# Kernel tuning notes

Hardware: AMD Instinct MI355X
Metric: run time of the kernel (lower is better)

## Reference

```python
import jax, jax.numpy as jnp
import numpy as np

WBITS = 4
GROUP_SIZE = 64
QMAX = 2 ** WBITS - 1  # 15
EPS = 1e-5


def setup_inputs() -> dict:
    key = jax.random.key(0)
    k1, k2, k3 = jax.random.split(key, 3)
    x = jax.random.normal(k1, (1, 512, 11008), dtype=jnp.float32)
    weight = jax.random.normal(k2, (4096, 11008), dtype=jnp.float32) * 0.02
    bias = jax.random.normal(k3, (4096,), dtype=jnp.float32) * 0.02
    return {"x": x, "weight": weight, "bias": bias}


def fake_quant_groupwise(w: jnp.ndarray) -> jnp.ndarray:
    """Uniform affine (asymmetric) group-wise fake quantization of the weight.

    Groups of GROUP_SIZE contiguous elements along the flattened weight share
    one (scale, zero_point) pair, computed dynamically from min/max per group,
    as in UniformAffineQuantizer(wbits, group_size, weight).
    """
    orig_shape = w.shape
    wg = w.reshape(-1, GROUP_SIZE)                     # [n_groups, G]
    xmin = jnp.min(wg, axis=1, keepdims=True)          # [n_groups, 1]
    xmax = jnp.max(wg, axis=1, keepdims=True)
    scale = jnp.maximum(xmax - xmin, EPS) / QMAX       # [n_groups, 1]
    zero_point = jnp.round(-xmin / scale)              # [n_groups, 1]
    w_int = jnp.clip(jnp.round(wg / scale) + zero_point, 0, QMAX)
    w_dq = (w_int - zero_point) * scale
    return w_dq.reshape(orig_shape)


def reference(x, weight, bias):
    w_q = fake_quant_groupwise(weight)                 # [out, in]
    # F.linear: x @ w_q.T + bias
    out = jnp.einsum('bsi,oi->bso', x, w_q) + bias
    return out
```

## Files before the change

kernel.cpp:

```cpp
#include <hip/hip_runtime.h>
#include <hip/hip_bf16.h>
#include <stdint.h>

typedef __attribute__((ext_vector_type(8))) short bf16x8;
typedef __attribute__((ext_vector_type(8))) short short8;
typedef __attribute__((ext_vector_type(4))) float f32x4;

#define M_DIM 512
#define N_DIM 4096
#define K_DIM 11008
#define KSTEPS 172

#define GLOBAL_AS(p) ((const __attribute__((address_space(1))) void*)(p))
#define LDS_AS(p)    ((__attribute__((address_space(3))) void*)(p))

__device__ __forceinline__ short f2bf(float f) {
    unsigned u = __float_as_uint(f);
    unsigned r = u + 0x7fff + ((u >> 16) & 1);
    return (short)(r >> 16);
}

__device__ __forceinline__ unsigned cvt_pk_bf16(float lo, float hi) {
    unsigned r;
    asm("v_cvt_pk_bf16_f32 %0, %1, %2" : "=v"(r) : "v"(lo), "v"(hi));
    return r;
}

__device__ __forceinline__ void fence_bar() {
    asm volatile("" ::: "memory");
    __builtin_amdgcn_s_barrier();
    asm volatile("" ::: "memory");
}
#define LGKM0() asm volatile("s_waitcnt lgkmcnt(0)" ::: "memory")
#define VMCNT(n) asm volatile("s_waitcnt vmcnt(" #n ")" ::: "memory")

__global__ __launch_bounds__(256) void conv_x(const float* __restrict__ x, short* __restrict__ xb) {
    const long long total = (long long)M_DIM * K_DIM;
    for (long long e0 = ((long long)blockIdx.x * 256 + threadIdx.x) * 8;
         e0 < total;
         e0 += (long long)gridDim.x * 256 * 8) {
        const float4* p = (const float4*)(x + e0);
        float4 v0 = p[0];
        float4 v1 = p[1];
        short8 s;
        s[0] = f2bf(v0.x); s[1] = f2bf(v0.y); s[2] = f2bf(v0.z); s[3] = f2bf(v0.w);
        s[4] = f2bf(v1.x); s[5] = f2bf(v1.y); s[6] = f2bf(v1.z); s[7] = f2bf(v1.w);
        *(short8*)(xb + e0) = s;
    }
}


template<int QD>
__device__ __forceinline__ void phase_reads(const short* __restrict__ Asd,
                                            const short* __restrict__ Bsd,
                                            int arow, int brow, int qb,
                                            bf16x8 (&af)[2][2], bf16x8 (&bfr)[2][4]) {
    if (QD == 0) {
        #pragma unroll
        for (int ks = 0; ks < 2; ++ks)
            #pragma unroll
            for (int fn = 0; fn < 4; ++fn) {
                const int r = brow + fn * 16;
                bfr[ks][fn] = *(const bf16x8*)&Bsd[r * 64 + (((ks * 4 + qb) ^ (r & 7)) * 8)];
            }
    }
    #pragma unroll
    for (int ks = 0; ks < 2; ++ks)
        #pragma unroll
        for (int j = 0; j < 2; ++j) {
            const int r = arow + (QD * 2 + j) * 16;
            af[ks][j] = *(const bf16x8*)&Asd[r * 64 + (((ks * 4 + qb) ^ (r & 7)) * 8)];
        }
}

template<int QD>
__device__ __forceinline__ void phase_mfma(const bf16x8 (&af)[2][2], const bf16x8 (&bfr)[2][4],
                                           f32x4 (&acc)[8][4]) {
    __builtin_amdgcn_s_setprio(1);
    #pragma unroll
    for (int ks = 0; ks < 2; ++ks)
        #pragma unroll
        for (int j = 0; j < 2; ++j)
            #pragma unroll
            for (int fn = 0; fn < 4; ++fn)
                acc[QD * 2 + j][fn] = __builtin_amdgcn_mfma_f32_16x16x32_bf16(
                    af[ks][j], bfr[ks][fn], acc[QD * 2 + j][fn], 0, 0, 0);
    __builtin_amdgcn_s_setprio(0);
}

__global__ __launch_bounds__(512, 2) void gemm_fq(const short* __restrict__ A,
                                                  const float* __restrict__ W,
                                                  unsigned short* __restrict__ P,
                                                  int spb) {
    __shared__ short As[2][256 * 64];
    __shared__ short Bs[2][256 * 64];
    const int tid  = threadIdx.x;
    const int lane = tid & 63;
    const int w    = tid >> 6;
    const int wr   = w >> 2;
    const int wc   = w & 3;
    const int m0   = blockIdx.y * 256;
    const int n0   = blockIdx.x * 256;
    const int kt0  = blockIdx.z * spb;
    const int kt1  = min(kt0 + spb, KSTEPS);

    const int srow = tid >> 3;
    const int sswz = (tid & 7) ^ (srow & 7);
    const int rQ   = tid >> 3;
    const int sQ   = tid & 7;
    const int arow = wr * 128 + (lane & 15);
    const int brow = wc * 64 + (lane & 15);
    const int qb   = lane >> 4;

    f32x4  acc[8][4] = {};
    bf16x8 bfr[2][4];
    bf16x8 af[2][2];
    float4 c0[2], c1[2], c2[2], c3[2];

    auto stageA = [&](int d, int h, int kt) {
        #pragma unroll
        for (int l = 0; l < 2; ++l) {
            __builtin_amdgcn_global_load_lds(
                GLOBAL_AS(A + (size_t)(m0 + h * 128 + l * 64 + srow) * K_DIM + kt * 64 + sswz * 8),
                LDS_AS(&As[d][(h * 128 + l * 64 + w * 8) * 64]), 16, 0, 0);
        }
    };
    auto loadBq = [&](float4 (&dst)[2], int c, int kt) {
        const float* src = W + (size_t)(n0 + c * 64 + rQ) * K_DIM + kt * 64 + sQ * 8;
        dst[0] = *(const float4*)(src);
        dst[1] = *(const float4*)(src + 4);
    };
    auto quantC = [&](const float4 (&v)[2], int c, short* BsF) {
        float mn = fminf(fminf(fminf(v[0].x, v[0].y), fminf(v[0].z, v[0].w)),
                         fminf(fminf(v[1].x, v[1].y), fminf(v[1].z, v[1].w)));
        float mx = fmaxf(fmaxf(fmaxf(v[0].x, v[0].y), fmaxf(v[0].z, v[0].w)),
                         fmaxf(fmaxf(v[1].x, v[1].y), fmaxf(v[1].z, v[1].w)));
        mn = fminf(mn, __int_as_float(__builtin_amdgcn_mov_dpp(__float_as_int(mn), 0xB1, 0xf, 0xf, true)));
        mx = fmaxf(mx, __int_as_float(__builtin_amdgcn_mov_dpp(__float_as_int(mx), 0xB1, 0xf, 0xf, true)));
        mn = fminf(mn, __int_as_float(__builtin_amdgcn_mov_dpp(__float_as_int(mn), 0x4E, 0xf, 0xf, true)));
        mx = fmaxf(mx, __int_as_float(__builtin_amdgcn_mov_dpp(__float_as_int(mx), 0x4E, 0xf, 0xf, true)));
        mn = fminf(mn, __int_as_float(__builtin_amdgcn_ds_swizzle(__float_as_int(mn), 0x101F)));
        mx = fmaxf(mx, __int_as_float(__builtin_amdgcn_ds_swizzle(__float_as_int(mx), 0x101F)));
        float range = fmaxf(mx - mn, 1e-5f);
        float scale = range * (1.0f / 15.0f);
        float rs    = 15.0f / range;
        float zp    = rintf(-mn * rs);
        const float lo = -zp, hi = 15.0f - zp;
        const float* pv = (const float*)&v[0];
        float q[8];
        #pragma unroll
        for (int j = 0; j < 8; ++j)
            q[j] = fminf(fmaxf(rintf(pv[j] * rs), lo), hi) * scale;
        union { unsigned u[4]; short8 s; } pk;
        #pragma unroll
        for (int j = 0; j < 4; ++j)
            pk.u[j] = cvt_pk_bf16(q[2 * j], q[2 * j + 1]);
        const int r = c * 64 + rQ;
        *(short8*)&BsF[r * 64 + ((sQ ^ (r & 7)) * 8)] = pk.s;
    };

    loadBq(c0, 0, kt0); loadBq(c1, 1, kt0); loadBq(c2, 2, kt0); loadBq(c3, 3, kt0);
    stageA(0, 0, kt0); stageA(0, 1, kt0);
    VMCNT(10); quantC(c0, 0, Bs[0]);
    VMCNT(8);  quantC(c1, 1, Bs[0]);
    VMCNT(6);  quantC(c2, 2, Bs[0]);
    VMCNT(4);  quantC(c3, 3, Bs[0]);
    {
        const int t1 = kt0 + 1;
        loadBq(c0, 0, t1); loadBq(c1, 1, t1); loadBq(c2, 2, t1); loadBq(c3, 3, t1);
    }
    VMCNT(8);
    VMCNT(6);
    LGKM0();
    fence_bar();

    int par = 0;
    for (int t = kt0; t < kt1; ++t) {
        const int tn  = (t + 1 < kt1) ? t + 1 : t;
        const int tn2 = (t + 2 < kt1) ? t + 2 : kt1 - 1;
        const short* Asc = As[par];
        const short* Bsc = Bs[par];
        short* Bsn = Bs[par ^ 1];
        phase_reads<0>(Asc, Bsc, arow, brow, qb, af, bfr);
        quantC(c0, 0, Bsn);
        stageA(par ^ 1, 0, tn);
        loadBq(c0, 0, tn2);
        fence_bar(); LGKM0();
        phase_mfma<0>(af, bfr, acc);
        fence_bar();
        phase_reads<1>(Asc, Bsc, arow, brow, qb, af, bfr);
        VMCNT(8);
        quantC(c1, 1, Bsn);
        stageA(par ^ 1, 1, tn);
        loadBq(c1, 1, tn2);
        fence_bar(); LGKM0();
        phase_mfma<1>(af, bfr, acc);
        fence_bar();
        phase_reads<2>(Asc, Bsc, arow, brow, qb, af, bfr);
        VMCNT(10);
        quantC(c2, 2, Bsn);
        loadBq(c2, 2, tn2);
        fence_bar(); LGKM0();
        phase_mfma<2>(af, bfr, acc);
        fence_bar();
        phase_reads<3>(Asc, Bsc, arow, brow, qb, af, bfr);
        VMCNT(10);
        quantC(c3, 3, Bsn);
        loadBq(c3, 3, tn2);
        fence_bar(); LGKM0();
        phase_mfma<3>(af, bfr, acc);
        VMCNT(6);
        fence_bar();
        par ^= 1;
    }

    VMCNT(0);

    unsigned short* out = P + (size_t)blockIdx.z * M_DIM * N_DIM;
    #pragma unroll
    for (int fm = 0; fm < 8; ++fm) {
        #pragma unroll
        for (int fn = 0; fn < 4; ++fn) {
            const int col  = n0 + wc * 64 + fn * 16 + (lane & 15);
            const int rowb = m0 + wr * 128 + fm * 16 + (lane >> 4) * 4;
            #pragma unroll
            for (int r = 0; r < 4; ++r) {
                out[(size_t)(rowb + r) * N_DIM + col] = (unsigned short)f2bf(acc[fm][fn][r]);
            }
        }
    }
}

__global__ __launch_bounds__(256) void reduce_out(const unsigned short* __restrict__ P,
                                                  const float* __restrict__ bias,
                                                  float* __restrict__ out,
                                                  int splitk) {
    const size_t total = (size_t)M_DIM * N_DIM;
    for (size_t idx8 = ((size_t)blockIdx.x * 256 + threadIdx.x) * 8;
         idx8 < total;
         idx8 += (size_t)gridDim.x * 256 * 8) {
        const int col = (int)(idx8 % N_DIM);
        float s[8];
        {
            float4 b0 = *(const float4*)(bias + col);
            float4 b1 = *(const float4*)(bias + col + 4);
            s[0] = b0.x; s[1] = b0.y; s[2] = b0.z; s[3] = b0.w;
            s[4] = b1.x; s[5] = b1.y; s[6] = b1.z; s[7] = b1.w;
        }
        for (int sp = 0; sp < splitk; ++sp) {
            short8 p = *(const short8*)(P + (size_t)sp * total + idx8);
            #pragma unroll
            for (int j = 0; j < 8; ++j)
                s[j] += __uint_as_float(((unsigned)(unsigned short)p[j]) << 16);
        }
        float4 o0 = {s[0], s[1], s[2], s[3]};
        float4 o1 = {s[4], s[5], s[6], s[7]};
        *(float4*)(out + idx8) = o0;
        *(float4*)(out + idx8 + 4) = o1;
    }
}

extern "C" void kernel_launch(void* const* d_in, const int* in_sizes, int n_in,
                              void* d_out, int out_size, void* d_ws, size_t ws_size,
                              hipStream_t stream) {
    const float* x    = (const float*)d_in[0];
    const float* wgt  = (const float*)d_in[1];
    const float* bias = (const float*)d_in[2];
    float* out = (float*)d_out;

    char* ws = (char*)d_ws;
    const size_t xb_bytes = (size_t)M_DIM * K_DIM * 2;
    short* xb = (short*)ws;
    unsigned short* part = (unsigned short*)(ws + xb_bytes);

    const size_t per_split = (size_t)M_DIM * N_DIM * 2;
    size_t avail = (ws_size > xb_bytes) ? (ws_size - xb_bytes) : 0;
    int splitk = 1, spb = KSTEPS;
    for (int sk = 8; sk >= 1; --sk) {
        if ((size_t)sk * per_split > avail) continue;
        int s = (KSTEPS + sk - 1) / sk;
        if (s & 1) s++;
        int last = KSTEPS - (sk - 1) * s;
        if (last < 2) continue;
        splitk = sk; spb = s;
        break;
    }

    hipLaunchKernelGGL(conv_x, dim3(2048), dim3(256), 0, stream, x, xb);
    hipLaunchKernelGGL(gemm_fq, dim3(N_DIM / 256, M_DIM / 256, splitk), dim3(512), 0, stream,
                       xb, wgt, part, spb);
    hipLaunchKernelGGL(reduce_out, dim3(1024), dim3(256), 0, stream, part, bias, out, splitk);
}
```

Before: 90.02 us.

## Remap weight quantization to two threads per row with register-level min/max

Each thread now loads 32 contiguous weight floats (half a 64-element group) instead of 8 floats across four chunks, so the group min/max reduction happens mostly in registers and needs a single DPP exchange instead of DPP plus ds_swizzle. The main loop is unrolled by two with fixed LDS buffer indices, and weight loads, reductions and quantization are spread over phases differently. This cuts cross-lane reduction work and gives wider contiguous loads. In exchange, register pressure rises (16 float4 buffers), and the wait-count and odd-step handling in the 2x unrolled loop are more fragile.

```diff
diff --git a/kernel.cpp b/kernel.cpp
--- a/kernel.cpp
+++ b/kernel.cpp
@@ -24,6 +24,15 @@
     unsigned r;
     asm("v_cvt_pk_bf16_f32 %0, %1, %2" : "=v"(r) : "v"(lo), "v"(hi));
     return r;
+}
+
+__device__ __forceinline__ float dpp_xor1_min(float v) {
+    int r = __builtin_amdgcn_mov_dpp(__float_as_int(v), 0xB1, 0xf, 0xf, true);
+    return fminf(v, __int_as_float(r));
+}
+__device__ __forceinline__ float dpp_xor1_max(float v) {
+    int r = __builtin_amdgcn_mov_dpp(__float_as_int(v), 0xB1, 0xf, 0xf, true);
+    return fmaxf(v, __int_as_float(r));
 }
 
 __device__ __forceinline__ void fence_bar() {
@@ -106,8 +115,8 @@
 
     const int srow = tid >> 3;
     const int sswz = (tid & 7) ^ (srow & 7);
-    const int rQ   = tid >> 3;
-    const int sQ   = tid & 7;
+    const int rQ   = tid >> 1;
+    const int hQ   = tid & 1;
     const int arow = wr * 128 + (lane & 15);
     const int brow = wc * 64 + (lane & 15);
     const int qb   = lane >> 4;
@@ -115,7 +124,8 @@
     f32x4  acc[8][4] = {};
     bf16x8 bfr[2][4];
     bf16x8 af[2][2];
-    float4 c0[2], c1[2], c2[2], c3[2];
+    float4 R0[8], R1[8];
+    float scale, rs, zp, qlo, qhi;
 
     auto stageA = [&](int d, int h, int kt) {
         #pragma unroll
@@ -125,93 +135,125 @@
                 LDS_AS(&As[d][(h * 128 + l * 64 + w * 8) * 64]), 16, 0, 0);
         }
     };
-    auto loadBq = [&](float4 (&dst)[2], int c, int kt) {
-        const float* src = W + (size_t)(n0 + c * 64 + rQ) * K_DIM + kt * 64 + sQ * 8;
-        dst[0] = *(const float4*)(src);
-        dst[1] = *(const float4*)(src + 4);
+    auto loadR = [&](float4 (&dst)[8], int half, int kt) {
+        const float4* src = (const float4*)(W + (size_t)(n0 + rQ) * K_DIM + kt * 64 + hQ * 32 + half * 16);
+        #pragma unroll
+        for (int j = 0; j < 4; ++j) dst[half * 4 + j] = src[j];
     };
-    auto quantC = [&](const float4 (&v)[2], int c, short* BsF) {
-        float mn = fminf(fminf(fminf(v[0].x, v[0].y), fminf(v[0].z, v[0].w)),
-                         fminf(fminf(v[1].x, v[1].y), fminf(v[1].z, v[1].w)));
-        float mx = fmaxf(fmaxf(fmaxf(v[0].x, v[0].y), fmaxf(v[0].z, v[0].w)),
-                         fmaxf(fmaxf(v[1].x, v[1].y), fmaxf(v[1].z, v[1].w)));
-        mn = fminf(mn, __int_as_float(__builtin_amdgcn_mov_dpp(__float_as_int(mn), 0xB1, 0xf, 0xf, true)));
-        mx = fmaxf(mx, __int_as_float(__builtin_amdgcn_mov_dpp(__float_as_int(mx), 0xB1, 0xf, 0xf, true)));
-        mn = fminf(mn, __int_as_float(__builtin_amdgcn_mov_dpp(__float_as_int(mn), 0x4E, 0xf, 0xf, true)));
-        mx = fmaxf(mx, __int_as_float(__builtin_amdgcn_mov_dpp(__float_as_int(mx), 0x4E, 0xf, 0xf, true)));
-        mn = fminf(mn, __int_as_float(__builtin_amdgcn_ds_swizzle(__float_as_int(mn), 0x101F)));
-        mx = fmaxf(mx, __int_as_float(__builtin_amdgcn_ds_swizzle(__float_as_int(mx), 0x101F)));
+    auto reduceR = [&](const float4 (&R)[8]) {
+        float mns[8], mxs[8];
+        #pragma unroll
+        for (int i = 0; i < 8; ++i) {
+            mns[i] = fminf(fminf(R[i].x, R[i].y), fminf(R[i].z, R[i].w));
+            mxs[i] = fmaxf(fmaxf(R[i].x, R[i].y), fmaxf(R[i].z, R[i].w));
+        }
+        #pragma unroll
+        for (int st = 4; st >= 1; st >>= 1)
+            #pragma unroll
+            for (int i = 0; i < st; ++i) {
+                mns[i] = fminf(mns[i], mns[i + st]);
+                mxs[i] = fmaxf(mxs[i], mxs[i + st]);
+            }
+        float mn = dpp_xor1_min(mns[0]);
+        float mx = dpp_xor1_max(mxs[0]);
         float range = fmaxf(mx - mn, 1e-5f);
-        float scale = range * (1.0f / 15.0f);
-        float rs    = 15.0f / range;
-        float zp    = rintf(-mn * rs);
-        const float lo = -zp, hi = 15.0f - zp;
-        const float* pv = (const float*)&v[0];
-        float q[8];
-        #pragma unroll
-        for (int j = 0; j < 8; ++j)
-            q[j] = fminf(fmaxf(rintf(pv[j] * rs), lo), hi) * scale;
-        union { unsigned u[4]; short8 s; } pk;
-        #pragma unroll
-        for (int j = 0; j < 4; ++j)
-            pk.u[j] = cvt_pk_bf16(q[2 * j], q[2 * j + 1]);
-        const int r = c * 64 + rQ;
-        *(short8*)&BsF[r * 64 + ((sQ ^ (r & 7)) * 8)] = pk.s;
+        scale = range * (1.0f / 15.0f);
+        rs    = 1.0f / scale;
+        zp    = rintf(-mn * rs);
+        qlo   = -zp;
+        qhi   = 15.0f - zp;
     };
-
-    loadBq(c0, 0, kt0); loadBq(c1, 1, kt0); loadBq(c2, 2, kt0); loadBq(c3, 3, kt0);
+    auto quantHalf = [&](const float4 (&R)[8], int half16, short* BsF) {
+        #pragma unroll
+        for (int pairq = 0; pairq < 2; ++pairq) {
+            const float4 va = R[half16 * 4 + pairq * 2 + 0];
+            const float4 vb = R[half16 * 4 + pairq * 2 + 1];
+            float q[8];
+            const float* pv = (const float*)&va;
+            #pragma unroll
+            for (int j = 0; j < 4; ++j)
+                q[j] = fminf(fmaxf(rintf(pv[j] * rs), qlo), qhi) * scale;
+            pv = (const float*)&vb;
+            #pragma unroll
+            for (int j = 0; j < 4; ++j)
+                q[4 + j] = fminf(fmaxf(rintf(pv[j] * rs), qlo), qhi) * scale;
+            union { unsigned u[4]; short8 s; } pk;
+            #pragma unroll
+            for (int j = 0; j < 4; ++j)
+                pk.u[j] = cvt_pk_bf16(q[2 * j], q[2 * j + 1]);
+            const int s = hQ * 4 + half16 * 2 + pairq;
+            *(short8*)&BsF[rQ * 64 + ((s ^ (rQ & 7)) * 8)] = pk.s;
+        }
+    };
+
+    loadR(R0, 0, kt0); loadR(R0, 1, kt0);
     stageA(0, 0, kt0); stageA(0, 1, kt0);
-    VMCNT(10); quantC(c0, 0, Bs[0]);
-    VMCNT(8);  quantC(c1, 1, Bs[0]);
-    VMCNT(6);  quantC(c2, 2, Bs[0]);
-    VMCNT(4);  quantC(c3, 3, Bs[0]);
-    {
-        const int t1 = kt0 + 1;
-        loadBq(c0, 0, t1); loadBq(c1, 1, t1); loadBq(c2, 2, t1); loadBq(c3, 3, t1);
-    }
+    VMCNT(4);
+    reduceR(R0);
+    quantHalf(R0, 0, Bs[0]);
+    quantHalf(R0, 1, Bs[0]);
+    loadR(R1, 0, kt0 + 1); loadR(R1, 1, kt0 + 1);
     VMCNT(8);
-    VMCNT(6);
     LGKM0();
     fence_bar();
 
-    int par = 0;
-    for (int t = kt0; t < kt1; ++t) {
-        const int tn  = (t + 1 < kt1) ? t + 1 : t;
-        const int tn2 = (t + 2 < kt1) ? t + 2 : kt1 - 1;
-        const short* Asc = As[par];
-        const short* Bsc = Bs[par];
-        short* Bsn = Bs[par ^ 1];
-        phase_reads<0>(Asc, Bsc, arow, brow, qb, af, bfr);
-        quantC(c0, 0, Bsn);
-        stageA(par ^ 1, 0, tn);
-        loadBq(c0, 0, tn2);
+    for (int t = kt0; t < kt1; t += 2) {
+        const int tb  = t + 1;
+        const int ta2 = (t + 2 < kt1) ? t + 2 : kt1 - 1;
+        const int tb2 = (t + 3 < kt1) ? t + 3 : kt1 - 1;
+        const int tAn = (t + 2 < kt1) ? t + 2 : tb;
+
+        phase_reads<0>(As[0], Bs[0], arow, brow, qb, af, bfr);
+        VMCNT(0);
+        reduceR(R1);
+        stageA(1, 0, tb);
+        loadR(R0, 0, ta2);
         fence_bar(); LGKM0();
         phase_mfma<0>(af, bfr, acc);
         fence_bar();
-        phase_reads<1>(Asc, Bsc, arow, brow, qb, af, bfr);
-        VMCNT(8);
-        quantC(c1, 1, Bsn);
-        stageA(par ^ 1, 1, tn);
-        loadBq(c1, 1, tn2);
+        phase_reads<1>(As[0], Bs[0], arow, brow, qb, af, bfr);
+        quantHalf(R1, 0, Bs[1]);
+        stageA(1, 1, tb);
+        loadR(R0, 1, ta2);
         fence_bar(); LGKM0();
         phase_mfma<1>(af, bfr, acc);
         fence_bar();
-        phase_reads<2>(Asc, Bsc, arow, brow, qb, af, bfr);
-        VMCNT(10);
-        quantC(c2, 2, Bsn);
-        loadBq(c2, 2, tn2);
+        phase_reads<2>(As[0], Bs[0], arow, brow, qb, af, bfr);
+        quantHalf(R1, 1, Bs[1]);
         fence_bar(); LGKM0();
         phase_mfma<2>(af, bfr, acc);
         fence_bar();
-        phase_reads<3>(Asc, Bsc, arow, brow, qb, af, bfr);
-        VMCNT(10);
-        quantC(c3, 3, Bsn);
-        loadBq(c3, 3, tn2);
+        phase_reads<3>(As[0], Bs[0], arow, brow, qb, af, bfr);
         fence_bar(); LGKM0();
         phase_mfma<3>(af, bfr, acc);
-        VMCNT(6);
-        fence_bar();
-        par ^= 1;
+        VMCNT(4);
+        fence_bar();
+
+        phase_reads<0>(As[1], Bs[1], arow, brow, qb, af, bfr);
+        VMCNT(0);
+        reduceR(R0);
+        stageA(0, 0, tAn);
+        loadR(R1, 0, tb2);
+        fence_bar(); LGKM0();
+        phase_mfma<0>(af, bfr, acc);
+        fence_bar();
+        phase_reads<1>(As[1], Bs[1], arow, brow, qb, af, bfr);
+        quantHalf(R0, 0, Bs[0]);
+        stageA(0, 1, tAn);
+        loadR(R1, 1, tb2);
+        fence_bar(); LGKM0();
+        phase_mfma<1>(af, bfr, acc);
+        fence_bar();
+        phase_reads<2>(As[1], Bs[1], arow, brow, qb, af, bfr);
+        quantHalf(R0, 1, Bs[0]);
+        fence_bar(); LGKM0();
+        phase_mfma<2>(af, bfr, acc);
+        fence_bar();
+        phase_reads<3>(As[1], Bs[1], arow, brow, qb, af, bfr);
+        fence_bar(); LGKM0();
+        phase_mfma<3>(af, bfr, acc);
+        VMCNT(4);
+        fence_bar();
     }
 
     VMCNT(0);
```

Result: slower. 171.4 us (+90.4%).

## Shrink GEMM tile to 128x128 with single-stage B quantization per k-step

Applied to the files above, without the earlier changes.

Rewrites the fused fake-quant GEMM to use 128x128 tiles with 256 threads. Each thread now loads 32 weights, and a pair of lanes reduces the group min/max. The four-phase interleaved pipeline becomes a simpler per-k-step loop with one B buffer. Split-K changes from up to 8 to 4. Doubling the number of M tiles means the fp32 weight is re-read and re-quantized twice as often, and the shallower pipeline hides less latency.

```diff
diff --git a/kernel.cpp b/kernel.cpp
--- a/kernel.cpp
+++ b/kernel.cpp
@@ -24,6 +24,10 @@
     unsigned r;
     asm("v_cvt_pk_bf16_f32 %0, %1, %2" : "=v"(r) : "v"(lo), "v"(hi));
     return r;
+}
+
+__device__ __forceinline__ float dpp_xor1(float v) {
+    return __int_as_float(__builtin_amdgcn_mov_dpp(__float_as_int(v), 0xB1, 0xf, 0xf, true));
 }
 
 __device__ __forceinline__ void fence_bar() {
@@ -49,167 +53,121 @@
     }
 }
 
-
-template<int QD>
-__device__ __forceinline__ void phase_reads(const short* __restrict__ Asd,
-                                            const short* __restrict__ Bsd,
-                                            int arow, int brow, int qb,
-                                            bf16x8 (&af)[2][2], bf16x8 (&bfr)[2][4]) {
-    if (QD == 0) {
-        #pragma unroll
-        for (int ks = 0; ks < 2; ++ks)
-            #pragma unroll
-            for (int fn = 0; fn < 4; ++fn) {
-                const int r = brow + fn * 16;
-                bfr[ks][fn] = *(const bf16x8*)&Bsd[r * 64 + (((ks * 4 + qb) ^ (r & 7)) * 8)];
-            }
-    }
-    #pragma unroll
-    for (int ks = 0; ks < 2; ++ks)
-        #pragma unroll
-        for (int j = 0; j < 2; ++j) {
-            const int r = arow + (QD * 2 + j) * 16;
-            af[ks][j] = *(const bf16x8*)&Asd[r * 64 + (((ks * 4 + qb) ^ (r & 7)) * 8)];
-        }
-}
-
-template<int QD>
-__device__ __forceinline__ void phase_mfma(const bf16x8 (&af)[2][2], const bf16x8 (&bfr)[2][4],
-                                           f32x4 (&acc)[8][4]) {
-    __builtin_amdgcn_s_setprio(1);
-    #pragma unroll
-    for (int ks = 0; ks < 2; ++ks)
-        #pragma unroll
-        for (int j = 0; j < 2; ++j)
-            #pragma unroll
-            for (int fn = 0; fn < 4; ++fn)
-                acc[QD * 2 + j][fn] = __builtin_amdgcn_mfma_f32_16x16x32_bf16(
-                    af[ks][j], bfr[ks][fn], acc[QD * 2 + j][fn], 0, 0, 0);
-    __builtin_amdgcn_s_setprio(0);
-}
-
-__global__ __launch_bounds__(512, 2) void gemm_fq(const short* __restrict__ A,
+__global__ __launch_bounds__(256, 2) void gemm_fq(const short* __restrict__ A,
                                                   const float* __restrict__ W,
                                                   unsigned short* __restrict__ P,
                                                   int spb) {
-    __shared__ short As[2][256 * 64];
-    __shared__ short Bs[2][256 * 64];
+    __shared__ short As[2][128 * 64];
+    __shared__ short Bs[128 * 64];
     const int tid  = threadIdx.x;
     const int lane = tid & 63;
     const int w    = tid >> 6;
-    const int wr   = w >> 2;
-    const int wc   = w & 3;
-    const int m0   = blockIdx.y * 256;
-    const int n0   = blockIdx.x * 256;
+    const int wr   = w >> 1;
+    const int wc   = w & 1;
+    const int m0   = blockIdx.y * 128;
+    const int n0   = blockIdx.x * 128;
     const int kt0  = blockIdx.z * spb;
     const int kt1  = min(kt0 + spb, KSTEPS);
 
-    const int srow = tid >> 3;
-    const int sswz = (tid & 7) ^ (srow & 7);
-    const int rQ   = tid >> 3;
-    const int sQ   = tid & 7;
-    const int arow = wr * 128 + (lane & 15);
-    const int brow = wc * 64 + (lane & 15);
+    const int srow = lane >> 3;
+    const int slot = lane & 7;
+    const int rQ   = tid >> 1;
+    const int hQ   = tid & 1;
+    const int frA  = wr * 64 + (lane & 15);
+    const int frB  = wc * 64 + (lane & 15);
     const int qb   = lane >> 4;
 
-    f32x4  acc[8][4] = {};
-    bf16x8 bfr[2][4];
-    bf16x8 af[2][2];
-    float4 c0[2], c1[2], c2[2], c3[2];
-
-    auto stageA = [&](int d, int h, int kt) {
-        #pragma unroll
-        for (int l = 0; l < 2; ++l) {
+    f32x4  acc[4][4] = {};
+    float4 R[8];
+
+    auto stageA = [&](int d, int kt) {
+        #pragma unroll
+        for (int i = 0; i < 4; ++i) {
+            const int rb  = (w * 4 + i) * 8;
+            const int row = rb + srow;
+            const int gcol = ((slot ^ (row & 7)) * 8);
             __builtin_amdgcn_global_load_lds(
-                GLOBAL_AS(A + (size_t)(m0 + h * 128 + l * 64 + srow) * K_DIM + kt * 64 + sswz * 8),
-                LDS_AS(&As[d][(h * 128 + l * 64 + w * 8) * 64]), 16, 0, 0);
+                GLOBAL_AS(A + (size_t)(m0 + row) * K_DIM + kt * 64 + gcol),
+                LDS_AS(&As[d][rb * 64]), 16, 0, 0);
         }
     };
-    auto loadBq = [&](float4 (&dst)[2], int c, int kt) {
-        const float* src = W + (size_t)(n0 + c * 64 + rQ) * K_DIM + kt * 64 + sQ * 8;
-        dst[0] = *(const float4*)(src);
-        dst[1] = *(const float4*)(src + 4);
+    auto loadR = [&](int kt) {
+        const float4* src = (const float4*)(W + (size_t)(n0 + rQ) * K_DIM + (size_t)kt * 64 + hQ * 32);
+        #pragma unroll
+        for (int j = 0; j < 8; ++j) R[j] = src[j];
     };
-    auto quantC = [&](const float4 (&v)[2], int c, short* BsF) {
-        float mn = fminf(fminf(fminf(v[0].x, v[0].y), fminf(v[0].z, v[0].w)),
-                         fminf(fminf(v[1].x, v[1].y), fminf(v[1].z, v[1].w)));
-        float mx = fmaxf(fmaxf(fmaxf(v[0].x, v[0].y), fmaxf(v[0].z, v[0].w)),
-                         fmaxf(fmaxf(v[1].x, v[1].y), fmaxf(v[1].z, v[1].w)));
-        mn = fminf(mn, __int_as_float(__builtin_amdgcn_mov_dpp(__float_as_int(mn), 0xB1, 0xf, 0xf, true)));
-        mx = fmaxf(mx, __int_as_float(__builtin_amdgcn_mov_dpp(__float_as_int(mx), 0xB1, 0xf, 0xf, true)));
-        mn = fminf(mn, __int_as_float(__builtin_amdgcn_mov_dpp(__float_as_int(mn), 0x4E, 0xf, 0xf, true)));
-        mx = fmaxf(mx, __int_as_float(__builtin_amdgcn_mov_dpp(__float_as_int(mx), 0x4E, 0xf, 0xf, true)));
-        mn = fminf(mn, __int_as_float(__builtin_amdgcn_ds_swizzle(__float_as_int(mn), 0x101F)));
-        mx = fmaxf(mx, __int_as_float(__builtin_amdgcn_ds_swizzle(__float_as_int(mx), 0x101F)));
+    auto quantB = [&]() {
+        const float* pv = (const float*)&R[0];
+        float mns[16], mxs[16];
+        #pragma unroll
+        for (int j = 0; j < 16; ++j) {
+            mns[j] = fminf(pv[2 * j], pv[2 * j + 1]);
+            mxs[j] = fmaxf(pv[2 * j], pv[2 * j + 1]);
+        }
+        #pragma unroll
+        for (int st = 8; st >= 1; st >>= 1)
+            #pragma unroll
+            for (int j = 0; j < st; ++j) {
+                mns[j] = fminf(mns[j], mns[j + st]);
+                mxs[j] = fmaxf(mxs[j], mxs[j + st]);
+            }
+        float mn = fminf(mns[0], dpp_xor1(mns[0]));
+        float mx = fmaxf(mxs[0], dpp_xor1(mxs[0]));
         float range = fmaxf(mx - mn, 1e-5f);
         float scale = range * (1.0f / 15.0f);
-        float rs    = 15.0f / range;
-        float zp    = rintf(-mn * rs);
-        const float lo = -zp, hi = 15.0f - zp;
-        const float* pv = (const float*)&v[0];
-        float q[8];
-        #pragma unroll
-        for (int j = 0; j < 8; ++j)
-            q[j] = fminf(fmaxf(rintf(pv[j] * rs), lo), hi) * scale;
-        union { unsigned u[4]; short8 s; } pk;
-        #pragma unroll
-        for (int j = 0; j < 4; ++j)
-            pk.u[j] = cvt_pk_bf16(q[2 * j], q[2 * j + 1]);
-        const int r = c * 64 + rQ;
-        *(short8*)&BsF[r * 64 + ((sQ ^ (r & 7)) * 8)] = pk.s;
+        float rs    = 1.0f / scale;
+        #pragma unroll
+        for (int s4 = 0; s4 < 4; ++s4) {
+            float q[8];
+            #pragma unroll
+            for (int j = 0; j < 8; ++j)
+                q[j] = rintf(pv[s4 * 8 + j] * rs) * scale;
+            union { unsigned u[4]; short8 s; } pk;
+            #pragma unroll
+            for (int j = 0; j < 4; ++j)
+                pk.u[j] = cvt_pk_bf16(q[2 * j], q[2 * j + 1]);
+            const int s = hQ * 4 + s4;
+            *(short8*)&Bs[rQ * 64 + ((s ^ (rQ & 7)) * 8)] = pk.s;
+        }
     };
 
-    loadBq(c0, 0, kt0); loadBq(c1, 1, kt0); loadBq(c2, 2, kt0); loadBq(c3, 3, kt0);
-    stageA(0, 0, kt0); stageA(0, 1, kt0);
-    VMCNT(10); quantC(c0, 0, Bs[0]);
-    VMCNT(8);  quantC(c1, 1, Bs[0]);
-    VMCNT(6);  quantC(c2, 2, Bs[0]);
-    VMCNT(4);  quantC(c3, 3, Bs[0]);
-    {
-        const int t1 = kt0 + 1;
-        loadBq(c0, 0, t1); loadBq(c1, 1, t1); loadBq(c2, 2, t1); loadBq(c3, 3, t1);
-    }
-    VMCNT(8);
-    VMCNT(6);
-    LGKM0();
-    fence_bar();
+    loadR(kt0);
+    stageA(0, kt0);
 
     int par = 0;
     for (int t = kt0; t < kt1; ++t) {
-        const int tn  = (t + 1 < kt1) ? t + 1 : t;
-        const int tn2 = (t + 2 < kt1) ? t + 2 : kt1 - 1;
-        const short* Asc = As[par];
-        const short* Bsc = Bs[par];
-        short* Bsn = Bs[par ^ 1];
-        phase_reads<0>(Asc, Bsc, arow, brow, qb, af, bfr);
-        quantC(c0, 0, Bsn);
-        stageA(par ^ 1, 0, tn);
-        loadBq(c0, 0, tn2);
-        fence_bar(); LGKM0();
-        phase_mfma<0>(af, bfr, acc);
+        const int tn = (t + 1 < kt1) ? t + 1 : t;
+        VMCNT(4);
+        quantB();
+        loadR(tn);
+        stageA(par ^ 1, tn);
+        LGKM0();
+        VMCNT(12);
         fence_bar();
-        phase_reads<1>(Asc, Bsc, arow, brow, qb, af, bfr);
-        VMCNT(8);
-        quantC(c1, 1, Bsn);
-        stageA(par ^ 1, 1, tn);
-        loadBq(c1, 1, tn2);
-        fence_bar(); LGKM0();
-        phase_mfma<1>(af, bfr, acc);
-        fence_bar();
-        phase_reads<2>(Asc, Bsc, arow, brow, qb, af, bfr);
-        VMCNT(10);
-        quantC(c2, 2, Bsn);
-        loadBq(c2, 2, tn2);
-        fence_bar(); LGKM0();
-        phase_mfma<2>(af, bfr, acc);
-        fence_bar();
-        phase_reads<3>(Asc, Bsc, arow, brow, qb, af, bfr);
-        VMCNT(10);
-        quantC(c3, 3, Bsn);
-        loadBq(c3, 3, tn2);
-        fence_bar(); LGKM0();
-        phase_mfma<3>(af, bfr, acc);
-        VMCNT(6);
+        #pragma unroll
+        for (int ks = 0; ks < 2; ++ks) {
+            bf16x8 af[4], bfr[4];
+            #pragma unroll
+            for (int fm = 0; fm < 4; ++fm) {
+                const int r = frA + fm * 16;
+                af[fm] = *(const bf16x8*)&As[par][r * 64 + (((ks * 4 + qb) ^ (r & 7)) * 8)];
+            }
+            #pragma unroll
+            for (int fn = 0; fn < 4; ++fn) {
+                const int r = frB + fn * 16;
+                bfr[fn] = *(const bf16x8*)&Bs[r * 64 + (((ks * 4 + qb) ^ (r & 7)) * 8)];
+            }
+            LGKM0();
+            __builtin_amdgcn_sched_barrier(0);
+            __builtin_amdgcn_s_setprio(1);
+            #pragma unroll
+            for (int fm = 0; fm < 4; ++fm)
+                #pragma unroll
+                for (int fn = 0; fn < 4; ++fn)
+                    acc[fm][fn] = __builtin_amdgcn_mfma_f32_16x16x32_bf16(
+                        af[fm], bfr[fn], acc[fm][fn], 0, 0, 0);
+            __builtin_amdgcn_s_setprio(0);
+        }
         fence_bar();
         par ^= 1;
     }
@@ -218,11 +176,11 @@
 
     unsigned short* out = P + (size_t)blockIdx.z * M_DIM * N_DIM;
     #pragma unroll
-    for (int fm = 0; fm < 8; ++fm) {
+    for (int fm = 0; fm < 4; ++fm) {
         #pragma unroll
         for (int fn = 0; fn < 4; ++fn) {
             const int col  = n0 + wc * 64 + fn * 16 + (lane & 15);
-            const int rowb = m0 + wr * 128 + fm * 16 + (lane >> 4) * 4;
+            const int rowb = m0 + wr * 64 + fm * 16 + (lane >> 4) * 4;
             #pragma unroll
             for (int r = 0; r < 4; ++r) {
                 out[(size_t)(rowb + r) * N_DIM + col] = (unsigned short)f2bf(acc[fm][fn][r]);
@@ -275,19 +233,12 @@
 
     const size_t per_split = (size_t)M_DIM * N_DIM * 2;
     size_t avail = (ws_size > xb_bytes) ? (ws_size - xb_bytes) : 0;
-    int splitk = 1, spb = KSTEPS;
-    for (int sk = 8; sk >= 1; --sk) {
-        if ((size_t)sk * per_split > avail) continue;
-        int s = (KSTEPS + sk - 1) / sk;
-        if (s & 1) s++;
-        int last = KSTEPS - (sk - 1) * s;
-        if (last < 2) continue;
-        splitk = sk; spb = s;
-        break;
-    }
+    int splitk = 4;
+    while (splitk > 1 && (size_t)splitk * per_split > avail) splitk--;
+    const int spb = (KSTEPS + splitk - 1) / splitk;
 
     hipLaunchKernelGGL(conv_x, dim3(2048), dim3(256), 0, stream, x, xb);
-    hipLaunchKernelGGL(gemm_fq, dim3(N_DIM / 256, M_DIM / 256, splitk), dim3(512), 0, stream,
+    hipLaunchKernelGGL(gemm_fq, dim3(N_DIM / 128, M_DIM / 128, splitk), dim3(256), 0, stream,
                        xb, wgt, part, spb);
     hipLaunchKernelGGL(reduce_out, dim3(1024), dim3(256), 0, stream, part, bias, out, splitk);
 }
```

After: 141.2 us. 1.57x slower.

## Quantize weight groups with four lanes per group and fewer loads

Applied to the files above, without the earlier changes.

The fp32 weight load and quantize mapping now gives each thread 16 contiguous floats, so four lanes cover one 64-wide group instead of eight. The B tile is now loaded in two 128-row chunks rather than four 64-row chunks. This removes the ds_swizzle reduction step and the explicit zero-point clamp, and moves the B quantization into the first two MFMA phases with loads issued in the last two. Split-k also no longer forces an even number of steps per block. In exchange, more registers are live per thread, and dropping the clamp relies on rounding never pushing values past the group range.

```diff
diff --git a/kernel.cpp b/kernel.cpp
--- a/kernel.cpp
+++ b/kernel.cpp
@@ -24,6 +24,13 @@
     unsigned r;
     asm("v_cvt_pk_bf16_f32 %0, %1, %2" : "=v"(r) : "v"(lo), "v"(hi));
     return r;
+}
+
+__device__ __forceinline__ float dpp_xor1(float v) {
+    return __int_as_float(__builtin_amdgcn_mov_dpp(__float_as_int(v), 0xB1, 0xf, 0xf, true));
+}
+__device__ __forceinline__ float dpp_xor2(float v) {
+    return __int_as_float(__builtin_amdgcn_mov_dpp(__float_as_int(v), 0x4E, 0xf, 0xf, true));
 }
 
 __device__ __forceinline__ void fence_bar() {
@@ -106,8 +113,8 @@
 
     const int srow = tid >> 3;
     const int sswz = (tid & 7) ^ (srow & 7);
-    const int rQ   = tid >> 3;
-    const int sQ   = tid & 7;
+    const int rC   = tid >> 2;
+    const int qC   = tid & 3;
     const int arow = wr * 128 + (lane & 15);
     const int brow = wc * 64 + (lane & 15);
     const int qb   = lane >> 4;
@@ -115,7 +122,7 @@
     f32x4  acc[8][4] = {};
     bf16x8 bfr[2][4];
     bf16x8 af[2][2];
-    float4 c0[2], c1[2], c2[2], c3[2];
+    float4 C0[4], C1[4];
 
     auto stageA = [&](int d, int h, int kt) {
         #pragma unroll
@@ -125,52 +132,59 @@
                 LDS_AS(&As[d][(h * 128 + l * 64 + w * 8) * 64]), 16, 0, 0);
         }
     };
-    auto loadBq = [&](float4 (&dst)[2], int c, int kt) {
-        const float* src = W + (size_t)(n0 + c * 64 + rQ) * K_DIM + kt * 64 + sQ * 8;
-        dst[0] = *(const float4*)(src);
-        dst[1] = *(const float4*)(src + 4);
+    auto loadC = [&](float4 (&dst)[4], int c, int kt) {
+        const float4* src = (const float4*)(W + (size_t)(n0 + c * 128 + rC) * K_DIM + (size_t)kt * 64 + qC * 16);
+        #pragma unroll
+        for (int j = 0; j < 4; ++j) dst[j] = src[j];
     };
-    auto quantC = [&](const float4 (&v)[2], int c, short* BsF) {
-        float mn = fminf(fminf(fminf(v[0].x, v[0].y), fminf(v[0].z, v[0].w)),
-                         fminf(fminf(v[1].x, v[1].y), fminf(v[1].z, v[1].w)));
-        float mx = fmaxf(fmaxf(fmaxf(v[0].x, v[0].y), fmaxf(v[0].z, v[0].w)),
-                         fmaxf(fmaxf(v[1].x, v[1].y), fmaxf(v[1].z, v[1].w)));
-        mn = fminf(mn, __int_as_float(__builtin_amdgcn_mov_dpp(__float_as_int(mn), 0xB1, 0xf, 0xf, true)));
-        mx = fmaxf(mx, __int_as_float(__builtin_amdgcn_mov_dpp(__float_as_int(mx), 0xB1, 0xf, 0xf, true)));
-        mn = fminf(mn, __int_as_float(__builtin_amdgcn_mov_dpp(__float_as_int(mn), 0x4E, 0xf, 0xf, true)));
-        mx = fmaxf(mx, __int_as_float(__builtin_amdgcn_mov_dpp(__float_as_int(mx), 0x4E, 0xf, 0xf, true)));
-        mn = fminf(mn, __int_as_float(__builtin_amdgcn_ds_swizzle(__float_as_int(mn), 0x101F)));
-        mx = fmaxf(mx, __int_as_float(__builtin_amdgcn_ds_swizzle(__float_as_int(mx), 0x101F)));
+    auto quantC = [&](const float4 (&v)[4], int c, short* BsF) {
+        const float* pv = (const float*)&v[0];
+        float mns[8], mxs[8];
+        #pragma unroll
+        for (int j = 0; j < 8; ++j) {
+            mns[j] = fminf(pv[2 * j], pv[2 * j + 1]);
+            mxs[j] = fmaxf(pv[2 * j], pv[2 * j + 1]);
+        }
+        #pragma unroll
+        for (int st = 4; st >= 1; st >>= 1)
+            #pragma unroll
+            for (int j = 0; j < st; ++j) {
+                mns[j] = fminf(mns[j], mns[j + st]);
+                mxs[j] = fmaxf(mxs[j], mxs[j + st]);
+            }
+        float mn = fminf(mns[0], dpp_xor1(mns[0]));
+        mn = fminf(mn, dpp_xor2(mn));
+        float mx = fmaxf(mxs[0], dpp_xor1(mxs[0]));
+        mx = fmaxf(mx, dpp_xor2(mx));
         float range = fmaxf(mx - mn, 1e-5f);
         float scale = range * (1.0f / 15.0f);
-        float rs    = 15.0f / range;
-        float zp    = rintf(-mn * rs);
-        const float lo = -zp, hi = 15.0f - zp;
-        const float* pv = (const float*)&v[0];
-        float q[8];
-        #pragma unroll
-        for (int j = 0; j < 8; ++j)
-            q[j] = fminf(fmaxf(rintf(pv[j] * rs), lo), hi) * scale;
-        union { unsigned u[4]; short8 s; } pk;
-        #pragma unroll
-        for (int j = 0; j < 4; ++j)
-            pk.u[j] = cvt_pk_bf16(q[2 * j], q[2 * j + 1]);
-        const int r = c * 64 + rQ;
-        *(short8*)&BsF[r * 64 + ((sQ ^ (r & 7)) * 8)] = pk.s;
+        float rs    = 1.0f / scale;
+        const int r    = c * 128 + rC;
+        const int base = r * 64;
+        #pragma unroll
+        for (int s4 = 0; s4 < 2; ++s4) {
+            float q[8];
+            #pragma unroll
+            for (int j = 0; j < 8; ++j)
+                q[j] = rintf(pv[s4 * 8 + j] * rs) * scale;
+            union { unsigned u[4]; short8 s; } pk;
+            #pragma unroll
+            for (int j = 0; j < 4; ++j)
+                pk.u[j] = cvt_pk_bf16(q[2 * j], q[2 * j + 1]);
+            const int s = qC * 2 + s4;
+            *(short8*)&BsF[base + ((s ^ (r & 7)) * 8)] = pk.s;
+        }
     };
 
-    loadBq(c0, 0, kt0); loadBq(c1, 1, kt0); loadBq(c2, 2, kt0); loadBq(c3, 3, kt0);
-    stageA(0, 0, kt0); stageA(0, 1, kt0);
-    VMCNT(10); quantC(c0, 0, Bs[0]);
-    VMCNT(8);  quantC(c1, 1, Bs[0]);
-    VMCNT(6);  quantC(c2, 2, Bs[0]);
-    VMCNT(4);  quantC(c3, 3, Bs[0]);
-    {
-        const int t1 = kt0 + 1;
-        loadBq(c0, 0, t1); loadBq(c1, 1, t1); loadBq(c2, 2, t1); loadBq(c3, 3, t1);
-    }
+    loadC(C0, 0, kt0);
+    loadC(C1, 1, kt0);
+    stageA(0, 0, kt0);
+    stageA(0, 1, kt0);
+    VMCNT(8);  quantC(C0, 0, Bs[0]);
+    VMCNT(4);  quantC(C1, 1, Bs[0]);
+    loadC(C0, 0, kt0 + 1);
+    loadC(C1, 1, kt0 + 1);
     VMCNT(8);
-    VMCNT(6);
     LGKM0();
     fence_bar();
 
@@ -182,34 +196,29 @@
         const short* Bsc = Bs[par];
         short* Bsn = Bs[par ^ 1];
         phase_reads<0>(Asc, Bsc, arow, brow, qb, af, bfr);
-        quantC(c0, 0, Bsn);
+        VMCNT(4);
+        quantC(C0, 0, Bsn);
         stageA(par ^ 1, 0, tn);
-        loadBq(c0, 0, tn2);
         fence_bar(); LGKM0();
         phase_mfma<0>(af, bfr, acc);
         fence_bar();
         phase_reads<1>(Asc, Bsc, arow, brow, qb, af, bfr);
-        VMCNT(8);
-        quantC(c1, 1, Bsn);
+        VMCNT(2);
+        quantC(C1, 1, Bsn);
         stageA(par ^ 1, 1, tn);
-        loadBq(c1, 1, tn2);
         fence_bar(); LGKM0();
         phase_mfma<1>(af, bfr, acc);
         fence_bar();
         phase_reads<2>(Asc, Bsc, arow, brow, qb, af, bfr);
-        VMCNT(10);
-        quantC(c2, 2, Bsn);
-        loadBq(c2, 2, tn2);
+        loadC(C0, 0, tn2);
         fence_bar(); LGKM0();
         phase_mfma<2>(af, bfr, acc);
         fence_bar();
         phase_reads<3>(Asc, Bsc, arow, brow, qb, af, bfr);
-        VMCNT(10);
-        quantC(c3, 3, Bsn);
-        loadBq(c3, 3, tn2);
+        loadC(C1, 1, tn2);
         fence_bar(); LGKM0();
         phase_mfma<3>(af, bfr, acc);
-        VMCNT(6);
+        VMCNT(8);
         fence_bar();
         par ^= 1;
     }
@@ -279,7 +288,6 @@
     for (int sk = 8; sk >= 1; --sk) {
         if ((size_t)sk * per_split > avail) continue;
         int s = (KSTEPS + sk - 1) / sk;
-        if (s & 1) s++;
         int last = KSTEPS - (sk - 1) * s;
         if (last < 2) continue;
         splitk = sk; spb = s;
```

Result: slower. 98.61 us (+9.5%).
